# Kernel tuning notes

Measured on AMD Instinct MI355X. Metric: run time of the kernel, lower is better.

The kernel has to match this reference:

```python
import jax, jax.numpy as jnp
import numpy as np

B = 65536        # batch_size
F = 128          # feature_dim (shared-layer output)
H = 256          # hidden dim of each domain tower
D = 8            # num_domains
OUT = 1          # per-domain tower output dim


def setup_inputs() -> dict:
    key = jax.random.key(0)
    k_x, k_w1, k_b1, k_w2, k_b2, k_id = jax.random.split(key, 6)
    x = jax.random.normal(k_x, (B, F), dtype=jnp.float32)
    select_domain_ids = jax.random.randint(k_id, (B,), 0, D)
    # stacked per-domain MLP params (one tower per domain)
    s1 = 1.0 / np.sqrt(F)
    s2 = 1.0 / np.sqrt(H)
    W1 = jax.random.uniform(k_w1, (D, F, H), minval=-s1, maxval=s1, dtype=jnp.float32)
    b1 = jax.random.uniform(k_b1, (D, H), minval=-s1, maxval=s1, dtype=jnp.float32)
    W2 = jax.random.uniform(k_w2, (D, H, OUT), minval=-s2, maxval=s2, dtype=jnp.float32)
    b2 = jax.random.uniform(k_b2, (D, OUT), minval=-s2, maxval=s2, dtype=jnp.float32)
    return {"x": x, "select_domain_ids": select_domain_ids,
            "W1": W1, "b1": b1, "W2": W2, "b2": b2}


def reference(x, select_domain_ids, W1, b1, W2, b2):
    # Run EVERY domain tower on the full batch (dense compute), as the
    # original module does, then gather the selected domain per sample.
    h = jax.nn.relu(jnp.einsum('bf,dfh->bdh', x, W1) + b1)      # [B, D, H]
    logits = jnp.einsum('bdh,dho->bdo', h, W2) + b2             # [B, D, OUT]
    # domain_select: logits[arange(B), domain_ids] -> [B, OUT]
    out = jnp.take_along_axis(logits, select_domain_ids[:, None, None], axis=1)[:, 0]
    return out
```

## Files before the change

kernel.cpp:

```cpp
#include <hip/hip_runtime.h>
#include <hip/hip_bf16.h>

#define BN 65536
#define FD 128
#define HD 256
#define DN 8
#define TM 64
#define SLOTS 8192
#define GRID_MAIN 2048

typedef float f32x4 __attribute__((ext_vector_type(4)));
using bf16x8 = __attribute__((ext_vector_type(8))) __bf16;
typedef unsigned short us4 __attribute__((ext_vector_type(4)));

__device__ __forceinline__ unsigned short f2bf(float f) {
  unsigned int x = __float_as_uint(f);
  x += 0x7fffu + ((x >> 16) & 1u);
  return (unsigned short)(x >> 16);
}

__global__ __launch_bounds__(256) void k_pre(
    const float* __restrict__ W1, const int* __restrict__ ids,
    unsigned short* __restrict__ W1T, int* __restrict__ g_cnt,
    int* __restrict__ perm) {
  __shared__ int hist[DN], base[DN];
  __shared__ unsigned short tile[64][136];
  int t = threadIdx.x, bid = blockIdx.x;

  if (t < DN) hist[t] = 0;
  __syncthreads();
  int i = bid * 256 + t;
  int id = ids[i];
  int lp = atomicAdd(&hist[id], 1);
  __syncthreads();
  if (t < DN) base[t] = atomicAdd(&g_cnt[t], hist[t]);
  __syncthreads();
  perm[(id << 16) + base[id] + lp] = i;

  if (bid < 32) {
    int db = bid >> 2, hb = bid & 3;
    int fr = t >> 4, hq = t & 15;
    const float* src = W1 + (size_t)db * FD * HD + hb * 64 + hq * 4;
#pragma unroll
    for (int jj = 0; jj < 8; jj++) {
      int f = fr + 16 * jj;
      f32x4 v = *(const f32x4*)(src + (size_t)f * HD);
#pragma unroll
      for (int e = 0; e < 4; e++) tile[hq * 4 + e][f] = f2bf(v[e]);
    }
    __syncthreads();
    unsigned short* dst = W1T + (size_t)db * HD * FD + (size_t)hb * 64 * FD;
    int h = t >> 2, c = t & 3;
#pragma unroll
    for (int j = 0; j < 4; j++) {
      int f = c * 32 + j * 8;
      *(us4*)(dst + h * FD + f)     = *(const us4*)&tile[h][f];
      *(us4*)(dst + h * FD + f + 4) = *(const us4*)&tile[h][f + 4];
    }
  }
}

__global__ __launch_bounds__(512, 4) void kmain(
    const float* __restrict__ x, const float* __restrict__ b1,
    const float* __restrict__ W2, const float* __restrict__ b2,
    const unsigned short* __restrict__ W1T, const int* __restrict__ perm,
    const int* __restrict__ g_cnt, float* __restrict__ out) {
  __shared__ unsigned short xs[TM * FD];
  __shared__ float s_red[TM][8];
  int t = threadIdx.x;

  for (int s = blockIdx.x; s < SLOTS; s += GRID_MAIN) {
    int d = s & 7, k = s >> 3;
    int rows = g_cnt[d] - k * TM;
    if (rows <= 0) continue;
    rows = min(rows, TM);
    const int* pr = perm + (d << 16) + k * TM;
    const unsigned short* Wd = W1T + (size_t)d * HD * FD;

    {
      int r = t >> 3, c8 = t & 7;
      int gi = pr[min(r, rows - 1)];
      const float* xr = x + (size_t)gi * FD;
      f32x4 v[4];
#pragma unroll
      for (int j = 0; j < 4; j++) v[j] = *(const f32x4*)(xr + (c8 + 8 * j) * 4);
#pragma unroll
      for (int j = 0; j < 4; j++) {
        int fc = c8 + 8 * j;
        int us = (r * FD + fc * 4) ^ ((r & 7) << 3);
        us4 wv;
        wv[0] = f2bf(v[j][0]); wv[1] = f2bf(v[j][1]);
        wv[2] = f2bf(v[j][2]); wv[3] = f2bf(v[j][3]);
        *(us4*)&xs[us] = wv;
      }
    }
    __syncthreads();

    int lane = t & 63, w = t >> 6;
    int lg = lane >> 4, lr = lane & 15;
    int colbase = w * 32;
    f32x4 acc[4][2];
#pragma unroll
    for (int mf = 0; mf < 4; mf++)
#pragma unroll
      for (int nt = 0; nt < 2; nt++) acc[mf][nt] = (f32x4){0.f, 0.f, 0.f, 0.f};

#pragma unroll
    for (int ks = 0; ks < 4; ks++) {
      bf16x8 a[4];
#pragma unroll
      for (int mf = 0; mf < 4; mf++) {
        int row = mf * 16 + lr;
        int us = (row * FD + ks * 32 + lg * 8) ^ ((row & 7) << 3);
        a[mf] = *(const bf16x8*)&xs[us];
      }
#pragma unroll
      for (int nt = 0; nt < 2; nt++) {
        int col = colbase + nt * 16 + lr;
        bf16x8 bfrag = *(const bf16x8*)(Wd + (size_t)col * FD + ks * 32 + lg * 8);
#pragma unroll
        for (int mf = 0; mf < 4; mf++)
          acc[mf][nt] = __builtin_amdgcn_mfma_f32_16x16x32_bf16(a[mf], bfrag, acc[mf][nt], 0, 0, 0);
      }
    }

    float part[4][4];
#pragma unroll
    for (int mf = 0; mf < 4; mf++)
#pragma unroll
      for (int q = 0; q < 4; q++) part[mf][q] = 0.f;
#pragma unroll
    for (int nt = 0; nt < 2; nt++) {
      int col = colbase + nt * 16 + lr;
      float b1v = b1[d * HD + col];
      float w2v = W2[d * HD + col];
#pragma unroll
      for (int mf = 0; mf < 4; mf++)
#pragma unroll
        for (int q = 0; q < 4; q++) {
          float h = acc[mf][nt][q] + b1v;
          h = h > 0.f ? h : 0.f;
          part[mf][q] = fmaf(h, w2v, part[mf][q]);
        }
    }
#pragma unroll
    for (int off = 1; off < 16; off <<= 1)
#pragma unroll
      for (int mf = 0; mf < 4; mf++)
#pragma unroll
        for (int q = 0; q < 4; q++)
          part[mf][q] += __shfl_xor(part[mf][q], off);
    if (lr == 0) {
#pragma unroll
      for (int mf = 0; mf < 4; mf++)
#pragma unroll
        for (int q = 0; q < 4; q++)
          s_red[mf * 16 + lg * 4 + q][w] = part[mf][q];
    }
    __syncthreads();
    if (t < rows) {
      const float* sr = s_red[t];
      out[pr[t]] = sr[0] + sr[1] + sr[2] + sr[3] + sr[4] + sr[5] + sr[6] + sr[7]
                   + b2[d];
    }
    __syncthreads();
  }
}

extern "C" void kernel_launch(void* const* d_in, const int* in_sizes, int n_in,
                              void* d_out, int out_size, void* d_ws, size_t ws_size,
                              hipStream_t stream) {
  const float* x   = (const float*)d_in[0];
  const int*   ids = (const int*)d_in[1];
  const float* W1  = (const float*)d_in[2];
  const float* b1  = (const float*)d_in[3];
  const float* W2  = (const float*)d_in[4];
  const float* b2  = (const float*)d_in[5];
  float* out = (float*)d_out;

  char* ws = (char*)d_ws;
  int* g_cnt = (int*)ws;
  int* perm  = (int*)(ws + 1024);
  unsigned short* W1T = (unsigned short*)(ws + 1024 + (size_t)DN * BN * 4);

  hipMemsetAsync(g_cnt, 0, DN * sizeof(int), stream);
  hipLaunchKernelGGL(k_pre, dim3(BN / 256), dim3(256), 0, stream,
                     W1, ids, W1T, g_cnt, perm);
  hipLaunchKernelGGL(kmain, dim3(GRID_MAIN), dim3(512), 0, stream,
                     x, b1, W2, b2, W1T, perm, g_cnt, out);
}
```

Baseline: 105.3 us.

## Replace atomic bucketing with block-prefix-scan and a compact tile list

The single bucketing kernel with global atomics and a memset is replaced by three kernels: per-block histograms plus W1 conversion, a single-block prefix scan that builds a compact list of non-empty (domain, tile) pairs, and a deterministic scatter into perm. The main kernel walks this compact tile list with a smaller grid instead of striding over all slots and skipping empty ones. It also preloads the W1 fragments, b1 and W2 into registers before the x staging, and pads s_red to avoid bank conflicts. The cost is two extra kernel launches, a serial single-block scan, and higher register pressure from holding the B fragments.

```diff
diff --git a/kernel.cpp b/kernel.cpp
--- a/kernel.cpp
+++ b/kernel.cpp
@@ -5,9 +5,9 @@
 #define FD 128
 #define HD 256
 #define DN 8
+#define NB 256
 #define TM 64
-#define SLOTS 8192
-#define GRID_MAIN 2048
+#define GRID_MAIN 1024
 
 typedef float f32x4 __attribute__((ext_vector_type(4)));
 using bf16x8 = __attribute__((ext_vector_type(8))) __bf16;
@@ -19,63 +19,123 @@
   return (unsigned short)(x >> 16);
 }
 
-__global__ __launch_bounds__(256) void k_pre(
+__global__ __launch_bounds__(256) void kA(
     const float* __restrict__ W1, const int* __restrict__ ids,
-    unsigned short* __restrict__ W1T, int* __restrict__ g_cnt,
+    unsigned short* __restrict__ W1T, int* __restrict__ cnt_blk) {
+  __shared__ int hist[DN];
+  __shared__ unsigned short tile[64][136];
+  int t = threadIdx.x, bid = blockIdx.x;
+  if (bid < NB) {
+    if (t < DN) hist[t] = 0;
+    __syncthreads();
+    atomicAdd(&hist[ids[bid * 256 + t]], 1);
+    __syncthreads();
+    if (t < DN) cnt_blk[bid * DN + t] = hist[t];
+  } else {
+    int db = (bid - NB) >> 2, hb = (bid - NB) & 3;
+    int fr = t >> 4, hq = t & 15;
+    const float* src = W1 + (size_t)db * FD * HD + hb * 64 + hq * 4;
+#pragma unroll
+    for (int jj = 0; jj < 8; jj++) {
+      int f = fr + 16 * jj;
+      f32x4 v = *(const f32x4*)(src + (size_t)f * HD);
+#pragma unroll
+      for (int e = 0; e < 4; e++) tile[hq * 4 + e][f] = f2bf(v[e]);
+    }
+    __syncthreads();
+    unsigned short* dst = W1T + (size_t)db * HD * FD + (size_t)hb * 64 * FD;
+    int h = t >> 2, c = t & 3;
+#pragma unroll
+    for (int j = 0; j < 4; j++) {
+      int f = c * 32 + j * 8;
+      *(us4*)(dst + h * FD + f)     = *(const us4*)&tile[h][f];
+      *(us4*)(dst + h * FD + f + 4) = *(const us4*)&tile[h][f + 4];
+    }
+  }
+}
+
+__global__ __launch_bounds__(512) void kB(
+    const int* __restrict__ cnt_blk, int* __restrict__ blk_base,
+    int* __restrict__ g_cnt, int* __restrict__ tile_list,
+    int* __restrict__ n_tiles) {
+  __shared__ int s_cnt[DN], s_T[DN + 1];
+  int t = threadIdx.x, d = t >> 6, l = t & 63;
+  int c[4], sum = 0;
+#pragma unroll
+  for (int j = 0; j < 4; j++) { c[j] = cnt_blk[(l * 4 + j) * DN + d]; sum += c[j]; }
+  int run = sum;
+  for (int off = 1; off < 64; off <<= 1) {
+    int v = __shfl_up(run, off);
+    if (l >= off) run += v;
+  }
+  int excl = run - sum;
+#pragma unroll
+  for (int j = 0; j < 4; j++) { blk_base[(l * 4 + j) * DN + d] = excl; excl += c[j]; }
+  if (l == 63) s_cnt[d] = run;
+  __syncthreads();
+  if (t == 0) {
+    int T = 0;
+    for (int dd = 0; dd < DN; dd++) {
+      g_cnt[dd] = s_cnt[dd];
+      s_T[dd] = T;
+      T += (s_cnt[dd] + TM - 1) / TM;
+    }
+    s_T[DN] = T;
+    *n_tiles = T;
+  }
+  __syncthreads();
+  int T = s_T[DN];
+  for (int tt = t; tt < T; tt += 512) {
+    int dd = 0;
+    while (s_T[dd + 1] <= tt) dd++;
+    tile_list[tt] = dd | ((tt - s_T[dd]) << 3);
+  }
+}
+
+__global__ __launch_bounds__(256) void kC(
+    const int* __restrict__ ids, const int* __restrict__ blk_base,
     int* __restrict__ perm) {
   __shared__ int hist[DN], base[DN];
-  __shared__ unsigned short tile[64][136];
   int t = threadIdx.x, bid = blockIdx.x;
-
-  if (t < DN) hist[t] = 0;
+  if (t < DN) { hist[t] = 0; base[t] = (t << 16) + blk_base[bid * DN + t]; }
   __syncthreads();
   int i = bid * 256 + t;
   int id = ids[i];
   int lp = atomicAdd(&hist[id], 1);
-  __syncthreads();
-  if (t < DN) base[t] = atomicAdd(&g_cnt[t], hist[t]);
-  __syncthreads();
-  perm[(id << 16) + base[id] + lp] = i;
-
-  if (bid < 32) {
-    int db = bid >> 2, hb = bid & 3;
-    int fr = t >> 4, hq = t & 15;
-    const float* src = W1 + (size_t)db * FD * HD + hb * 64 + hq * 4;
-#pragma unroll
-    for (int jj = 0; jj < 8; jj++) {
-      int f = fr + 16 * jj;
-      f32x4 v = *(const f32x4*)(src + (size_t)f * HD);
-#pragma unroll
-      for (int e = 0; e < 4; e++) tile[hq * 4 + e][f] = f2bf(v[e]);
-    }
-    __syncthreads();
-    unsigned short* dst = W1T + (size_t)db * HD * FD + (size_t)hb * 64 * FD;
-    int h = t >> 2, c = t & 3;
-#pragma unroll
-    for (int j = 0; j < 4; j++) {
-      int f = c * 32 + j * 8;
-      *(us4*)(dst + h * FD + f)     = *(const us4*)&tile[h][f];
-      *(us4*)(dst + h * FD + f + 4) = *(const us4*)&tile[h][f + 4];
-    }
-  }
+  perm[base[id] + lp] = i;
 }
 
 __global__ __launch_bounds__(512, 4) void kmain(
     const float* __restrict__ x, const float* __restrict__ b1,
     const float* __restrict__ W2, const float* __restrict__ b2,
     const unsigned short* __restrict__ W1T, const int* __restrict__ perm,
-    const int* __restrict__ g_cnt, float* __restrict__ out) {
+    const int* __restrict__ g_cnt, const int* __restrict__ tile_list,
+    const int* __restrict__ n_tiles, float* __restrict__ out) {
   __shared__ unsigned short xs[TM * FD];
-  __shared__ float s_red[TM][8];
+  __shared__ float s_red[TM][9];
+  int T = *n_tiles;
   int t = threadIdx.x;
-
-  for (int s = blockIdx.x; s < SLOTS; s += GRID_MAIN) {
-    int d = s & 7, k = s >> 3;
-    int rows = g_cnt[d] - k * TM;
-    if (rows <= 0) continue;
-    rows = min(rows, TM);
+  int lane = t & 63, w = t >> 6;
+  int lg = lane >> 4, lr = lane & 15;
+
+  for (int i = blockIdx.x; i < T; i += GRID_MAIN) {
+    int info = tile_list[i];
+    int d = info & 7, k = info >> 3;
+    int rows = min(g_cnt[d] - k * TM, TM);
     const int* pr = perm + (d << 16) + k * TM;
     const unsigned short* Wd = W1T + (size_t)d * HD * FD;
+
+    float b1v[2], w2v[2];
+    bf16x8 bfr[4][2];
+#pragma unroll
+    for (int nt = 0; nt < 2; nt++) {
+      int col = w * 32 + nt * 16 + lr;
+      b1v[nt] = b1[d * HD + col];
+      w2v[nt] = W2[d * HD + col];
+#pragma unroll
+      for (int ks = 0; ks < 4; ks++)
+        bfr[ks][nt] = *(const bf16x8*)(Wd + (size_t)col * FD + ks * 32 + lg * 8);
+    }
 
     {
       int r = t >> 3, c8 = t & 7;
@@ -96,9 +156,6 @@
     }
     __syncthreads();
 
-    int lane = t & 63, w = t >> 6;
-    int lg = lane >> 4, lr = lane & 15;
-    int colbase = w * 32;
     f32x4 acc[4][2];
 #pragma unroll
     for (int mf = 0; mf < 4; mf++)
@@ -115,13 +172,10 @@
         a[mf] = *(const bf16x8*)&xs[us];
       }
 #pragma unroll
-      for (int nt = 0; nt < 2; nt++) {
-        int col = colbase + nt * 16 + lr;
-        bf16x8 bfrag = *(const bf16x8*)(Wd + (size_t)col * FD + ks * 32 + lg * 8);
+      for (int nt = 0; nt < 2; nt++)
 #pragma unroll
         for (int mf = 0; mf < 4; mf++)
-          acc[mf][nt] = __builtin_amdgcn_mfma_f32_16x16x32_bf16(a[mf], bfrag, acc[mf][nt], 0, 0, 0);
-      }
+          acc[mf][nt] = __builtin_amdgcn_mfma_f32_16x16x32_bf16(a[mf], bfr[ks][nt], acc[mf][nt], 0, 0, 0);
     }
 
     float part[4][4];
@@ -130,19 +184,15 @@
 #pragma unroll
       for (int q = 0; q < 4; q++) part[mf][q] = 0.f;
 #pragma unroll
-    for (int nt = 0; nt < 2; nt++) {
-      int col = colbase + nt * 16 + lr;
-      float b1v = b1[d * HD + col];
-      float w2v = W2[d * HD + col];
+    for (int nt = 0; nt < 2; nt++)
 #pragma unroll
       for (int mf = 0; mf < 4; mf++)
 #pragma unroll
         for (int q = 0; q < 4; q++) {
-          float h = acc[mf][nt][q] + b1v;
+          float h = acc[mf][nt][q] + b1v[nt];
           h = h > 0.f ? h : 0.f;
-          part[mf][q] = fmaf(h, w2v, part[mf][q]);
+          part[mf][q] = fmaf(h, w2v[nt], part[mf][q]);
         }
-    }
 #pragma unroll
     for (int off = 1; off < 16; off <<= 1)
 #pragma unroll
@@ -178,14 +228,19 @@
   const float* b2  = (const float*)d_in[5];
   float* out = (float*)d_out;
 
-  char* ws = (char*)d_ws;
-  int* g_cnt = (int*)ws;
-  int* perm  = (int*)(ws + 1024);
-  unsigned short* W1T = (unsigned short*)(ws + 1024 + (size_t)DN * BN * 4);
-
-  hipMemsetAsync(g_cnt, 0, DN * sizeof(int), stream);
-  hipLaunchKernelGGL(k_pre, dim3(BN / 256), dim3(256), 0, stream,
-                     W1, ids, W1T, g_cnt, perm);
-  hipLaunchKernelGGL(kmain, dim3(GRID_MAIN), dim3(512), 0, stream,
-                     x, b1, W2, b2, W1T, perm, g_cnt, out);
-}
+  int* ws_i = (int*)d_ws;
+  int* g_cnt     = ws_i;
+  int* n_tiles   = ws_i + 16;
+  int* cnt_blk   = ws_i + 64;
+  int* blk_base  = ws_i + 2112;
+  int* tile_list = ws_i + 4160;
+  int* perm      = ws_i + 8192;
+  unsigned short* W1T = (unsigned short*)(ws_i + 8192 + DN * BN);
+
+  hipLaunchKernelGGL(kA, dim3(NB + 32), dim3(256), 0, stream, W1, ids, W1T, cnt_blk);
+  hipLaunchKernelGGL(kB, dim3(1), dim3(512), 0, stream, cnt_blk, blk_base, g_cnt,
+                     tile_list, n_tiles);
+  hipLaunchKernelGGL(kC, dim3(NB), dim3(256), 0, stream, ids, blk_base, perm);
+  hipLaunchKernelGGL(kmain, dim3(GRID_MAIN), dim3(512), 0, stream, x, b1, W2, b2,
+                     W1T, perm, g_cnt, tile_list, n_tiles, out);
+}
```

After: 102.7 us. -2.5%, faster.
